# Performance work log

Measured on AMD Instinct MI355X. Metric: run time of the kernel, lower is better.

Reference implementation:

```python
import jax, jax.numpy as jnp
import numpy as np

VX, VY = 0.16, 0.16
PC = (0.0, -39.68, -3.0, 69.12, 39.68, 1.0)
X_OFFSET = VX / 2 + PC[0]
Y_OFFSET = VY / 2 + PC[1]
X_L = int((PC[3] - PC[0]) / VX)   # 432
Y_L = int((PC[4] - PC[1]) / VY)   # 496
C = 64
BN_EPS = 1e-3
LN_EPS = 1e-5


def setup_inputs() -> dict:
    key = jax.random.key(0)
    ks = jax.random.split(key, 16)
    B, PPB, M = 4, 10000, 32
    P = B * PPB
    # unique (x,y) pillar coords per batch, sorted by batch index (matches per-batch loop order)
    rng = np.random.default_rng(0)
    coords = []
    for i in range(B):
        lin = rng.choice(X_L * Y_L, PPB, replace=False)
        coords.append(np.stack([np.full(PPB, i), lin // Y_L, lin % Y_L], axis=1))
    coors_batch = jnp.asarray(np.concatenate(coords, axis=0), dtype=jnp.int32)
    npoints_per_pillar = jax.random.randint(ks[0], (P,), 1, M + 1, dtype=jnp.int32)
    lo = jnp.array([0.5, -39.68, -3.0, 0.0], jnp.float32)
    hi = jnp.array([69.12, 39.68, 1.0, 1.0], jnp.float32)
    pts = lo + jax.random.uniform(ks[1], (P, M, 4), dtype=jnp.float32) * (hi - lo)
    valid = (jnp.arange(M)[None, :] < npoints_per_pillar[:, None])[:, :, None]
    pillars = pts * valid  # zero-padded beyond npoints, as real voxelizers produce
    H_IMG, W_IMG = 192, 640  # half-resolution image feature map
    batch_image_map = jax.random.normal(ks[2], (B, C, H_IMG, W_IMG), dtype=jnp.float32)
    # pinhole-style 3x4 projection with forward-x as depth: u=(cx*x - fx*y)/x, v=(cy*x - fy*z)/x
    fx, fy, cx, cy = 700.0, 700.0, 640.0, 192.0
    calib = jnp.array([[cx, -fx, 0.0, 0.0], [cy, 0.0, -fy, 0.0], [1.0, 0.0, 0.0, 0.0]], jnp.float32)
    batched_calibs = jnp.tile(calib[None], (B, 1, 1)) * (1.0 + 0.01 * jax.random.normal(ks[3], (B, 3, 4)))
    conv_w = 0.1 * jax.random.normal(ks[4], (C, 9), dtype=jnp.float32)
    bn_gamma = 1.0 + 0.1 * jax.random.normal(ks[5], (C,), dtype=jnp.float32)
    bn_beta = 0.1 * jax.random.normal(ks[6], (C,), dtype=jnp.float32)
    bn_mean = 0.1 * jax.random.normal(ks[7], (C,), dtype=jnp.float32)
    bn_var = jax.random.uniform(ks[8], (C,), minval=0.5, maxval=1.5, dtype=jnp.float32)
    g_w1 = 0.1 * jax.random.normal(ks[9], (2 * C, 2 * C), dtype=jnp.float32)
    g_b1 = 0.1 * jax.random.normal(ks[10], (2 * C,), dtype=jnp.float32)
    ln_gamma = 1.0 + 0.1 * jax.random.normal(ks[11], (2 * C,), dtype=jnp.float32)
    ln_beta = 0.1 * jax.random.normal(ks[12], (2 * C,), dtype=jnp.float32)
    g_w2 = 0.1 * jax.random.normal(ks[13], (C, 2 * C), dtype=jnp.float32)
    g_b2 = 0.1 * jax.random.normal(ks[14], (C,), dtype=jnp.float32)
    return dict(pillars=pillars, coors_batch=coors_batch, npoints_per_pillar=npoints_per_pillar,
                batch_image_map=batch_image_map, batched_calibs=batched_calibs, batch_size=B,
                conv_w=conv_w, bn_gamma=bn_gamma, bn_beta=bn_beta, bn_mean=bn_mean, bn_var=bn_var,
                g_w1=g_w1, g_b1=g_b1, ln_gamma=ln_gamma, ln_beta=ln_beta, g_w2=g_w2, g_b2=g_b2)


def reference(pillars, coors_batch, npoints_per_pillar, batch_image_map, batched_calibs, batch_size,
              conv_w, bn_gamma, bn_beta, bn_mean, bn_var, g_w1, g_b1, ln_gamma, ln_beta, g_w2, g_b2):
    P, M, _ = pillars.shape
    npts = npoints_per_pillar.astype(pillars.dtype)
    mean_center = jnp.sum(pillars[:, :, :3], axis=1, keepdims=True) / npts[:, None, None]  # [P,1,3]
    offset_pt_center = pillars[:, :, :3] - mean_center
    cx = coors_batch[:, None, 1:2].astype(pillars.dtype) * VX + X_OFFSET
    cy = coors_batch[:, None, 2:3].astype(pillars.dtype) * VY + Y_OFFSET
    x_off = pillars[:, :, 0:1] - cx
    y_off = pillars[:, :, 1:2] - cy
    # channels 0,1 of the original concat are overwritten with x_off,y_off in-place
    features = jnp.concatenate([x_off, y_off, pillars[:, :, 2:], offset_pt_center, x_off, y_off], axis=-1)  # [P,M,9]
    mask = jnp.arange(M)[None, :] < npoints_per_pillar[:, None]
    features = features * mask[:, :, None]
    # Conv1d(k=1, no bias) + BatchNorm1d(eval) + ReLU (double ReLU in source collapses to one)
    h = jnp.einsum('pmi,ci->pmc', features, conv_w)
    h = (h - bn_mean) * (bn_gamma / jnp.sqrt(bn_var + BN_EPS)) + bn_beta
    h = jax.nn.relu(h)
    pooling_features = jnp.max(h, axis=1)  # [P,C]
    # vectorized image-feature gather (coors sorted by batch idx, so order matches the per-batch loop)
    bidx = coors_batch[:, 0]
    ctr = mean_center[:, 0, :]  # [P,3]
    hom = jnp.concatenate([ctr, jnp.ones((P, 1), ctr.dtype)], axis=-1)  # [P,4]
    proj = jnp.einsum('pij,pj->pi', batched_calibs[bidx], hom)
    depth = proj[:, 2]
    u = proj[:, 0] / depth
    v = proj[:, 1] / depth
    h_img, w_img = batch_image_map.shape[2], batch_image_map.shape[3]
    u = jnp.clip(u / 2, 0, w_img - 1).astype(jnp.int32)
    v = jnp.clip(v / 2, 0, h_img - 1).astype(jnp.int32)
    image_features = batch_image_map.transpose(0, 2, 3, 1)[bidx, v, u]  # [P,C]
    # gated fusion
    cat = jnp.concatenate([pooling_features, image_features], axis=1)  # [P,2C]
    g = cat @ g_w1.T + g_b1
    mu = jnp.mean(g, axis=-1, keepdims=True)
    var = jnp.var(g, axis=-1, keepdims=True)
    g = (g - mu) / jnp.sqrt(var + LN_EPS) * ln_gamma + ln_beta
    g = jax.nn.relu(g)
    gate = jax.nn.sigmoid(g @ g_w2.T + g_b2)  # [P,C]
    gate_features = pooling_features * gate + image_features * (1.0 - gate)
    # scatter to dense BEV canvas [B, x_l, y_l, C] then permute to [B, C, y_l, x_l]
    canvas = jnp.zeros((batch_size, X_L, Y_L, C), dtype=jnp.float32)
    canvas = canvas.at[bidx, coors_batch[:, 1], coors_batch[:, 2]].set(gate_features)
    return canvas.transpose(0, 3, 2, 1)
```

## Files before the change

kernel.cpp:

```cpp
#include <hip/hip_runtime.h>
#include <cfloat>
#include <cmath>

#define XL 432
#define YL 496
#define NCH 64
#define HIMG 192
#define WIMG 640
#define HW (HIMG * WIMG)
#define PTS_M 32

#define WAVES 16
#define TPB (WAVES * 64)
#define PPG 4
#define NBLOCKS 256
#define WPITCH 132

typedef const __attribute__((address_space(1))) void* gas_t;
typedef __attribute__((address_space(3))) void* las_t;

__device__ __forceinline__ void gload_lds16(const float* g, float* l) {
    __builtin_amdgcn_global_load_lds((gas_t)g, (las_t)l, 16, 0, 0);
}

#define RED5(v) { v += __shfl_xor(v, 16); v += __shfl_xor(v, 8); v += __shfl_xor(v, 4); \
                  v += __shfl_xor(v, 2);  v += __shfl_xor(v, 1); }

__global__ void zerofill(float4* __restrict__ o, int n4) {
    int i = blockIdx.x * blockDim.x + threadIdx.x;
    const int st = gridDim.x * blockDim.x;
    const float4 z = make_float4(0.f, 0.f, 0.f, 0.f);
    for (; i < n4; i += st) o[i] = z;
}

__global__ __launch_bounds__(256) void transpose_cl(
    const float* __restrict__ img, float* __restrict__ imgT)
{
    __shared__ float t[64 * 257];
    const int b    = blockIdx.x / (HW / 256);
    const int tile = blockIdx.x % (HW / 256);
    const int hw0  = tile * 256;
    const int tid  = threadIdx.x;

    const float* base = img + (size_t)b * NCH * HW + hw0;
    #pragma unroll 4
    for (int c = 0; c < 64; ++c)
        t[c * 257 + tid] = base[(size_t)c * HW + tid];
    __syncthreads();

    float* ob = imgT + ((size_t)b * HW + hw0) * NCH;
    const int c = tid & 63, r = tid >> 6;
    #pragma unroll 4
    for (int it = 0; it < 64; ++it) {
        const int hw = it * 4 + r;
        ob[hw * 64 + c] = t[c * 257 + hw];
    }
}

template<int MODE>
__global__ __launch_bounds__(TPB, 4) void pillar_compute(
    const float* __restrict__ pillars, const int* __restrict__ coors,
    const int* __restrict__ npp, const float* __restrict__ image,
    const float* __restrict__ calibs, const float* __restrict__ conv_w,
    const float* __restrict__ bng, const float* __restrict__ bnb,
    const float* __restrict__ bnm, const float* __restrict__ bnv,
    const float* __restrict__ w1, const float* __restrict__ b1,
    const float* __restrict__ lng, const float* __restrict__ lnb,
    const float* __restrict__ w2, const float* __restrict__ b2,
    float* __restrict__ feat, int* __restrict__ idxmap,
    float* __restrict__ out, int P)
{
    __shared__ float w1p[128 * WPITCH];
    __shared__ float w2p[64 * WPITCH];
    __shared__ float ws[WAVES][512];

    const int tid  = threadIdx.x;
    const int lane = tid & 63;
    const int wv   = tid >> 6;

    for (int i = tid; i < 128 * 32; i += TPB) {
        const int j = i >> 5, k4 = i & 31;
        ((float4*)(w1p + j * WPITCH))[k4] = ((const float4*)w1)[i];
    }
    for (int i = tid; i < 64 * 32; i += TPB) {
        const int j = i >> 5, k4 = i & 31;
        ((float4*)(w2p + j * WPITCH))[k4] = ((const float4*)w2)[i];
    }
    __syncthreads();

    float cw[9];
    #pragma unroll
    for (int i = 0; i < 9; ++i) cw[i] = conv_w[lane * 9 + i];
    const float s   = bng[lane] / sqrtf(bnv[lane] + 1e-3f);
    const float tch = bnb[lane] - bnm[lane] * s;
    const float As  = (cw[0] + cw[4] + cw[7]) * s;
    const float Bs  = (cw[1] + cw[5] + cw[8]) * s;
    const float Cs  = (cw[2] + cw[6]) * s;
    const float Ds  = cw[3] * s;
    const float w07 = (cw[0] + cw[7]) * s;
    const float w18 = (cw[1] + cw[8]) * s;
    const float w4s = cw[4] * s, w5s = cw[5] * s, w6s = cw[6] * s;

    const float b1a = b1[lane], b1b = b1[lane + 64];
    const float lga = lng[lane], lgb = lng[lane + 64];
    const float lba = lnb[lane], lbb = lnb[lane + 64];
    const float gb2 = b2[lane];

    float* wsw = ws[wv];
    const float4* wsf4 = (const float4*)wsw;
    const float4* w1rA = (const float4*)(w1p + lane * WPITCH);
    const float4* w1rB = (const float4*)(w1p + (lane + 64) * WPITCH);
    const float4* w2r  = (const float4*)(w2p + lane * WPITCH);

    const int ntasks = (P + PPG - 1) / PPG;

    for (int grp = blockIdx.x * WAVES + wv; grp < ntasks; grp += NBLOCKS * WAVES) {
        const int pbase = grp * PPG;
        const bool full = (pbase + PPG <= P);

        asm volatile("s_waitcnt lgkmcnt(0)" ::: "memory");
        if (full) {
            const float* src = pillars + (size_t)pbase * (PTS_M * 4);
            gload_lds16(src + lane * 4, wsw);
            gload_lds16(src + 256 + lane * 4, wsw + 256);
        } else {
            #pragma unroll
            for (int h = 0; h < 2; ++h) {
                const int idx = pbase * PTS_M + h * 64 + lane;
                float4 v = make_float4(0.f, 0.f, 0.f, 0.f);
                if (idx < P * PTS_M) v = ((const float4*)pillars)[idx];
                ((float4*)wsw)[h * 64 + lane] = v;
            }
        }

        int bbv[PPG], ixv[PPG], iyv[PPG], nv[PPG];
        #pragma unroll
        for (int pp = 0; pp < PPG; ++pp) {
            const int p = pbase + pp;
            if (p < P) {
                bbv[pp] = coors[p * 3]; ixv[pp] = coors[p * 3 + 1];
                iyv[pp] = coors[p * 3 + 2]; nv[pp] = npp[p];
            } else { bbv[pp] = 0; ixv[pp] = 0; iyv[pp] = 0; nv[pp] = 1; }
        }

        asm volatile("s_waitcnt vmcnt(0) lgkmcnt(0)" ::: "memory");

        const float4 qa = wsf4[lane];
        const float4 qb = wsf4[64 + lane];
        float ax = qa.x, ay = qa.y, az = qa.z;
        float bx = qb.x, by = qb.y, bz = qb.z;
        RED5(ax) RED5(ay) RED5(az)
        RED5(bx) RED5(by) RED5(bz)
        const float axo = __shfl_xor(ax, 32), ayo = __shfl_xor(ay, 32), azo = __shfl_xor(az, 32);
        const float bxo = __shfl_xor(bx, 32), byo = __shfl_xor(by, 32), bzo = __shfl_xor(bz, 32);
        const bool lo = lane < 32;
        float mx[PPG], my[PPG], mz[PPG];
        {
            const float f0 = 1.f / (float)nv[0], f1 = 1.f / (float)nv[1];
            const float f2 = 1.f / (float)nv[2], f3 = 1.f / (float)nv[3];
            mx[0] = (lo ? ax : axo) * f0;  mx[1] = (lo ? axo : ax) * f1;
            my[0] = (lo ? ay : ayo) * f0;  my[1] = (lo ? ayo : ay) * f1;
            mz[0] = (lo ? az : azo) * f0;  mz[1] = (lo ? azo : az) * f1;
            mx[2] = (lo ? bx : bxo) * f2;  mx[3] = (lo ? bxo : bx) * f3;
            my[2] = (lo ? by : byo) * f2;  my[3] = (lo ? byo : by) * f3;
            mz[2] = (lo ? bz : bzo) * f2;  mz[3] = (lo ? bzo : bz) * f3;
        }

        float img[PPG], Es[PPG];
        #pragma unroll
        for (int pp = 0; pp < PPG; ++pp) {
            const float* cb = calibs + bbv[pp] * 12;
            const float pr0 = cb[0]*mx[pp] + cb[1]*my[pp] + cb[2]*mz[pp] + cb[3];
            const float pr1 = cb[4]*mx[pp] + cb[5]*my[pp] + cb[6]*mz[pp] + cb[7];
            const float pr2 = cb[8]*mx[pp] + cb[9]*my[pp] + cb[10]*mz[pp] + cb[11];
            float uf = (pr0 / pr2) * 0.5f;
            float vf = (pr1 / pr2) * 0.5f;
            uf = fminf(fmaxf(uf, 0.f), (float)(WIMG - 1));
            vf = fminf(fmaxf(vf, 0.f), (float)(HIMG - 1));
            const int u = (int)uf, v = (int)vf;
            if (MODE == 2) {
                img[pp] = image[((size_t)bbv[pp] * HW + (size_t)v * WIMG + u) * NCH + lane];
            } else {
                img[pp] = image[(((size_t)(bbv[pp] * NCH + lane)) * HIMG + v) * WIMG + u];
            }
            const float cxp = (float)ixv[pp] * 0.16f + 0.08f;
            const float cyp = (float)iyv[pp] * 0.16f + (-39.6f);
            Es[pp] = tch - (cxp * w07 + cyp * w18 + mx[pp] * w4s + my[pp] * w5s + mz[pp] * w6s);
        }

        float pooled[PPG];
        #pragma unroll
        for (int pp = 0; pp < PPG; ++pp) {
            const int n = nv[pp];
            float p0 = (n < PTS_M) ? tch : -FLT_MAX;
            float p1 = -FLT_MAX, p2 = -FLT_MAX, p3 = -FLT_MAX;
            #pragma unroll
            for (int m = 0; m < PTS_M; m += 4) {
                const float4 q0 = wsf4[pp * 32 + m];
                const float4 q1 = wsf4[pp * 32 + m + 1];
                const float4 q2 = wsf4[pp * 32 + m + 2];
                const float4 q3 = wsf4[pp * 32 + m + 3];
                const float h0 = Es[pp] + q0.x*As + q0.y*Bs + q0.z*Cs + q0.w*Ds;
                const float h1 = Es[pp] + q1.x*As + q1.y*Bs + q1.z*Cs + q1.w*Ds;
                const float h2 = Es[pp] + q2.x*As + q2.y*Bs + q2.z*Cs + q2.w*Ds;
                const float h3 = Es[pp] + q3.x*As + q3.y*Bs + q3.z*Cs + q3.w*Ds;
                p0 = fmaxf(p0, (m     < n) ? h0 : -FLT_MAX);
                p1 = fmaxf(p1, (m + 1 < n) ? h1 : -FLT_MAX);
                p2 = fmaxf(p2, (m + 2 < n) ? h2 : -FLT_MAX);
                p3 = fmaxf(p3, (m + 3 < n) ? h3 : -FLT_MAX);
            }
            pooled[pp] = fmaxf(fmaxf(fmaxf(p0, p1), fmaxf(p2, p3)), 0.f);
        }

        #pragma unroll
        for (int pp = 0; pp < PPG; ++pp) {
            wsw[pp * 128 + lane]      = pooled[pp];
            wsw[pp * 128 + 64 + lane] = img[pp];
        }
        asm volatile("s_waitcnt lgkmcnt(0)" ::: "memory");

        float accA[PPG], accB[PPG];
        #pragma unroll
        for (int pp = 0; pp < PPG; ++pp) { accA[pp] = b1a; accB[pp] = b1b; }
        #pragma unroll 4
        for (int k4 = 0; k4 < 32; ++k4) {
            const float4 wa = w1rA[k4];
            const float4 wb = w1rB[k4];
            #pragma unroll
            for (int pp = 0; pp < PPG; ++pp) {
                const float4 cv = wsf4[pp * 32 + k4];
                accA[pp] += cv.x*wa.x + cv.y*wa.y + cv.z*wa.z + cv.w*wa.w;
                accB[pp] += cv.x*wb.x + cv.y*wb.y + cv.z*wb.z + cv.w*wb.w;
            }
        }

        float sum[PPG], sq[PPG];
        #pragma unroll
        for (int pp = 0; pp < PPG; ++pp) {
            sum[pp] = accA[pp] + accB[pp];
            sq[pp]  = accA[pp]*accA[pp] + accB[pp]*accB[pp];
        }
        #pragma unroll
        for (int d = 32; d; d >>= 1) {
            #pragma unroll
            for (int pp = 0; pp < PPG; ++pp) {
                sum[pp] += __shfl_xor(sum[pp], d);
                sq[pp]  += __shfl_xor(sq[pp], d);
            }
        }
        #pragma unroll
        for (int pp = 0; pp < PPG; ++pp) {
            const float mu  = sum[pp] * (1.f / 128.f);
            const float var = sq[pp] * (1.f / 128.f) - mu * mu;
            const float inv = 1.f / sqrtf(var + 1e-5f);
            const float g0 = (accA[pp] - mu) * inv * lga + lba;
            const float g1 = (accB[pp] - mu) * inv * lgb + lbb;
            wsw[pp * 128 + lane]      = fmaxf(g0, 0.f);
            wsw[pp * 128 + 64 + lane] = fmaxf(g1, 0.f);
        }
        asm volatile("s_waitcnt lgkmcnt(0)" ::: "memory");

        float ac2[PPG];
        #pragma unroll
        for (int pp = 0; pp < PPG; ++pp) ac2[pp] = gb2;
        #pragma unroll 4
        for (int k4 = 0; k4 < 32; ++k4) {
            const float4 w = w2r[k4];
            #pragma unroll
            for (int pp = 0; pp < PPG; ++pp) {
                const float4 gv = wsf4[pp * 32 + k4];
                ac2[pp] += gv.x*w.x + gv.y*w.y + gv.z*w.z + gv.w*w.w;
            }
        }
        #pragma unroll
        for (int pp = 0; pp < PPG; ++pp) {
            const int p = pbase + pp;
            if (p >= P) continue;
            const float gate = 1.f / (1.f + expf(-ac2[pp]));
            const float gf = pooled[pp] * gate + img[pp] * (1.f - gate);
            if (MODE == 0) {
                out[(((bbv[pp] * NCH) + lane) * YL + iyv[pp]) * XL + ixv[pp]] = gf;
            } else {
                feat[(size_t)p * NCH + lane] = gf;
                if (lane == 0)
                    idxmap[(bbv[pp] * YL + iyv[pp]) * XL + ixv[pp]] = p + 1;
            }
        }
    }
}

__global__ __launch_bounds__(256) void canvas_build(
    const float* __restrict__ feat, const int* __restrict__ idxmap,
    float4* __restrict__ out)
{
    __shared__ int idxrow[XL];
    const int by = blockIdx.x;
    const int b = by / YL, y = by % YL;
    const int* irow = idxmap + (size_t)by * XL;
    for (int i = threadIdx.x; i < XL; i += 256) idxrow[i] = irow[i];
    __syncthreads();

    const int NF4 = XL / 4;
    for (int t = threadIdx.x; t < NCH * NF4; t += 256) {
        const int c = t / NF4, x4 = t - c * NF4;
        const int i0 = idxrow[x4*4+0], i1 = idxrow[x4*4+1];
        const int i2 = idxrow[x4*4+2], i3 = idxrow[x4*4+3];
        float4 o = make_float4(0.f, 0.f, 0.f, 0.f);
        if (i0) o.x = feat[(size_t)(i0-1) * NCH + c];
        if (i1) o.y = feat[(size_t)(i1-1) * NCH + c];
        if (i2) o.z = feat[(size_t)(i2-1) * NCH + c];
        if (i3) o.w = feat[(size_t)(i3-1) * NCH + c];
        out[((size_t)(b * NCH + c) * YL + y) * NF4 + x4] = o;
    }
}

extern "C" void kernel_launch(void* const* d_in, const int* in_sizes, int n_in,
                              void* d_out, int out_size, void* d_ws, size_t ws_size,
                              hipStream_t stream)
{
    const float* pillars = (const float*)d_in[0];
    const int*   coors   = (const int*)d_in[1];
    const int*   npp     = (const int*)d_in[2];
    const float* image   = (const float*)d_in[3];
    const float* calibs  = (const float*)d_in[4];
    const float* conv_w  = (const float*)d_in[6];
    const float* bng     = (const float*)d_in[7];
    const float* bnb     = (const float*)d_in[8];
    const float* bnm     = (const float*)d_in[9];
    const float* bnv     = (const float*)d_in[10];
    const float* w1      = (const float*)d_in[11];
    const float* b1      = (const float*)d_in[12];
    const float* lng     = (const float*)d_in[13];
    const float* lnb     = (const float*)d_in[14];
    const float* w2      = (const float*)d_in[15];
    const float* b2      = (const float*)d_in[16];
    float* out = (float*)d_out;
    const int P = in_sizes[0] / (PTS_M * 4);
    const int B = in_sizes[3] / (NCH * HW);

    const size_t featBytes = (size_t)P * NCH * sizeof(float);
    const size_t idxBytes  = (size_t)B * YL * XL * sizeof(int);
    const size_t imgTBytes = (size_t)B * HW * NCH * sizeof(float);

    if (ws_size >= featBytes + idxBytes + imgTBytes) {
        float* feat   = (float*)d_ws;
        int*   idxmap = (int*)((char*)d_ws + featBytes);
        float* imgT   = (float*)((char*)d_ws + featBytes + idxBytes);
        zerofill<<<dim3(880), dim3(256), 0, stream>>>((float4*)idxmap, (int)(idxBytes / 16));
        transpose_cl<<<dim3(B * (HW / 256)), dim3(256), 0, stream>>>(image, imgT);
        pillar_compute<2><<<dim3(NBLOCKS), dim3(TPB), 0, stream>>>(
            pillars, coors, npp, imgT, calibs, conv_w, bng, bnb, bnm, bnv,
            w1, b1, lng, lnb, w2, b2, feat, idxmap, nullptr, P);
        canvas_build<<<dim3(B * YL), dim3(256), 0, stream>>>(feat, idxmap, (float4*)d_out);
    } else if (ws_size >= featBytes + idxBytes) {
        float* feat   = (float*)d_ws;
        int*   idxmap = (int*)((char*)d_ws + featBytes);
        zerofill<<<dim3(880), dim3(256), 0, stream>>>((float4*)idxmap, (int)(idxBytes / 16));
        pillar_compute<1><<<dim3(NBLOCKS), dim3(TPB), 0, stream>>>(
            pillars, coors, npp, image, calibs, conv_w, bng, bnb, bnm, bnv,
            w1, b1, lng, lnb, w2, b2, feat, idxmap, nullptr, P);
        canvas_build<<<dim3(B * YL), dim3(256), 0, stream>>>(feat, idxmap, (float4*)d_out);
    } else {
        zerofill<<<dim3(2048), dim3(256), 0, stream>>>((float4*)d_out, out_size / 4);
        pillar_compute<0><<<dim3(NBLOCKS), dim3(TPB), 0, stream>>>(
            pillars, coors, npp, image, calibs, conv_w, bng, bnb, bnm, bnv,
            w1, b1, lng, lnb, w2, b2, nullptr, nullptr, out, P);
    }
}
```

Measured before the change: 210.5 us.

## Fuse zerofill, transpose, pillar compute and canvas build into one cooperative kernel

```diff
diff --git a/kernel.cpp b/kernel.cpp
--- a/kernel.cpp
+++ b/kernel.cpp
@@ -1,6 +1,9 @@
 #include <hip/hip_runtime.h>
+#include <hip/hip_cooperative_groups.h>
 #include <cfloat>
 #include <cmath>
+
+namespace cg = cooperative_groups;
 
 #define XL 432
 #define YL 496
@@ -26,6 +29,335 @@
 #define RED5(v) { v += __shfl_xor(v, 16); v += __shfl_xor(v, 8); v += __shfl_xor(v, 4); \
                   v += __shfl_xor(v, 2);  v += __shfl_xor(v, 1); }
 
+
+struct ChanConst {
+    float As, Bs, Cs, Ds, w07, w18, w4s, w5s, w6s, tch;
+    float b1a, b1b, lga, lgb, lba, lbb, gb2;
+};
+
+__device__ __forceinline__ ChanConst load_chan_consts(
+    int lane, const float* conv_w, const float* bng, const float* bnb,
+    const float* bnm, const float* bnv, const float* b1, const float* lng,
+    const float* lnb, const float* b2)
+{
+    ChanConst cc;
+    float cw[9];
+    #pragma unroll
+    for (int i = 0; i < 9; ++i) cw[i] = conv_w[lane * 9 + i];
+    const float s = bng[lane] / sqrtf(bnv[lane] + 1e-3f);
+    cc.tch = bnb[lane] - bnm[lane] * s;
+    cc.As  = (cw[0] + cw[4] + cw[7]) * s;
+    cc.Bs  = (cw[1] + cw[5] + cw[8]) * s;
+    cc.Cs  = (cw[2] + cw[6]) * s;
+    cc.Ds  = cw[3] * s;
+    cc.w07 = (cw[0] + cw[7]) * s;
+    cc.w18 = (cw[1] + cw[8]) * s;
+    cc.w4s = cw[4] * s; cc.w5s = cw[5] * s; cc.w6s = cw[6] * s;
+    cc.b1a = b1[lane];  cc.b1b = b1[lane + 64];
+    cc.lga = lng[lane]; cc.lgb = lng[lane + 64];
+    cc.lba = lnb[lane]; cc.lbb = lnb[lane + 64];
+    cc.gb2 = b2[lane];
+    return cc;
+}
+
+template<int MODE>
+__device__ __forceinline__ void pillar_group(
+    int grp, int P, int lane, float* wsw,
+    const float* __restrict__ pillars, const int* __restrict__ coors,
+    const int* __restrict__ npp, const float* __restrict__ image,
+    const float* __restrict__ calibs, const ChanConst& cc,
+    const float4* w1rA, const float4* w1rB, const float4* w2r,
+    float* __restrict__ feat, int* __restrict__ idxmap, float* __restrict__ out)
+{
+    const float4* wsf4 = (const float4*)wsw;
+    const int pbase = grp * PPG;
+    const bool full = (pbase + PPG <= P);
+
+    asm volatile("s_waitcnt lgkmcnt(0)" ::: "memory");
+    if (full) {
+        const float* src = pillars + (size_t)pbase * (PTS_M * 4);
+        gload_lds16(src + lane * 4, wsw);
+        gload_lds16(src + 256 + lane * 4, wsw + 256);
+    } else {
+        #pragma unroll
+        for (int h = 0; h < 2; ++h) {
+            const int idx = pbase * PTS_M + h * 64 + lane;
+            float4 v = make_float4(0.f, 0.f, 0.f, 0.f);
+            if (idx < P * PTS_M) v = ((const float4*)pillars)[idx];
+            ((float4*)wsw)[h * 64 + lane] = v;
+        }
+    }
+
+    int bbv[PPG], ixv[PPG], iyv[PPG], nv[PPG];
+    #pragma unroll
+    for (int pp = 0; pp < PPG; ++pp) {
+        const int p = pbase + pp;
+        if (p < P) {
+            bbv[pp] = coors[p * 3]; ixv[pp] = coors[p * 3 + 1];
+            iyv[pp] = coors[p * 3 + 2]; nv[pp] = npp[p];
+        } else { bbv[pp] = 0; ixv[pp] = 0; iyv[pp] = 0; nv[pp] = 1; }
+    }
+
+    asm volatile("s_waitcnt vmcnt(0) lgkmcnt(0)" ::: "memory");
+
+    const float4 qa = wsf4[lane];
+    const float4 qb = wsf4[64 + lane];
+    float ax = qa.x, ay = qa.y, az = qa.z;
+    float bx = qb.x, by = qb.y, bz = qb.z;
+    RED5(ax) RED5(ay) RED5(az)
+    RED5(bx) RED5(by) RED5(bz)
+    const float axo = __shfl_xor(ax, 32), ayo = __shfl_xor(ay, 32), azo = __shfl_xor(az, 32);
+    const float bxo = __shfl_xor(bx, 32), byo = __shfl_xor(by, 32), bzo = __shfl_xor(bz, 32);
+    const bool lo = lane < 32;
+    float mx[PPG], my[PPG], mz[PPG];
+    {
+        const float f0 = 1.f / (float)nv[0], f1 = 1.f / (float)nv[1];
+        const float f2 = 1.f / (float)nv[2], f3 = 1.f / (float)nv[3];
+        mx[0] = (lo ? ax : axo) * f0;  mx[1] = (lo ? axo : ax) * f1;
+        my[0] = (lo ? ay : ayo) * f0;  my[1] = (lo ? ayo : ay) * f1;
+        mz[0] = (lo ? az : azo) * f0;  mz[1] = (lo ? azo : az) * f1;
+        mx[2] = (lo ? bx : bxo) * f2;  mx[3] = (lo ? bxo : bx) * f3;
+        my[2] = (lo ? by : byo) * f2;  my[3] = (lo ? byo : by) * f3;
+        mz[2] = (lo ? bz : bzo) * f2;  mz[3] = (lo ? bzo : bz) * f3;
+    }
+
+    float img[PPG], Es[PPG];
+    #pragma unroll
+    for (int pp = 0; pp < PPG; ++pp) {
+        const float* cb = calibs + bbv[pp] * 12;
+        const float pr0 = cb[0]*mx[pp] + cb[1]*my[pp] + cb[2]*mz[pp] + cb[3];
+        const float pr1 = cb[4]*mx[pp] + cb[5]*my[pp] + cb[6]*mz[pp] + cb[7];
+        const float pr2 = cb[8]*mx[pp] + cb[9]*my[pp] + cb[10]*mz[pp] + cb[11];
+        float uf = (pr0 / pr2) * 0.5f;
+        float vf = (pr1 / pr2) * 0.5f;
+        uf = fminf(fmaxf(uf, 0.f), (float)(WIMG - 1));
+        vf = fminf(fmaxf(vf, 0.f), (float)(HIMG - 1));
+        const int u = (int)uf, v = (int)vf;
+        if (MODE == 2) {
+            img[pp] = image[((size_t)bbv[pp] * HW + (size_t)v * WIMG + u) * NCH + lane];
+        } else {
+            img[pp] = image[(((size_t)(bbv[pp] * NCH + lane)) * HIMG + v) * WIMG + u];
+        }
+        const float cxp = (float)ixv[pp] * 0.16f + 0.08f;
+        const float cyp = (float)iyv[pp] * 0.16f + (-39.6f);
+        Es[pp] = cc.tch - (cxp * cc.w07 + cyp * cc.w18 + mx[pp] * cc.w4s + my[pp] * cc.w5s + mz[pp] * cc.w6s);
+    }
+
+    float pooled[PPG];
+    #pragma unroll
+    for (int pp = 0; pp < PPG; ++pp) {
+        const int n = nv[pp];
+        float p0 = (n < PTS_M) ? cc.tch : -FLT_MAX;
+        float p1 = -FLT_MAX, p2 = -FLT_MAX, p3 = -FLT_MAX;
+        #pragma unroll
+        for (int m = 0; m < PTS_M; m += 4) {
+            const float4 q0 = wsf4[pp * 32 + m];
+            const float4 q1 = wsf4[pp * 32 + m + 1];
+            const float4 q2 = wsf4[pp * 32 + m + 2];
+            const float4 q3 = wsf4[pp * 32 + m + 3];
+            const float h0 = Es[pp] + q0.x*cc.As + q0.y*cc.Bs + q0.z*cc.Cs + q0.w*cc.Ds;
+            const float h1 = Es[pp] + q1.x*cc.As + q1.y*cc.Bs + q1.z*cc.Cs + q1.w*cc.Ds;
+            const float h2 = Es[pp] + q2.x*cc.As + q2.y*cc.Bs + q2.z*cc.Cs + q2.w*cc.Ds;
+            const float h3 = Es[pp] + q3.x*cc.As + q3.y*cc.Bs + q3.z*cc.Cs + q3.w*cc.Ds;
+            p0 = fmaxf(p0, (m     < n) ? h0 : -FLT_MAX);
+            p1 = fmaxf(p1, (m + 1 < n) ? h1 : -FLT_MAX);
+            p2 = fmaxf(p2, (m + 2 < n) ? h2 : -FLT_MAX);
+            p3 = fmaxf(p3, (m + 3 < n) ? h3 : -FLT_MAX);
+        }
+        pooled[pp] = fmaxf(fmaxf(fmaxf(p0, p1), fmaxf(p2, p3)), 0.f);
+    }
+
+    #pragma unroll
+    for (int pp = 0; pp < PPG; ++pp) {
+        wsw[pp * 128 + lane]      = pooled[pp];
+        wsw[pp * 128 + 64 + lane] = img[pp];
+    }
+    asm volatile("s_waitcnt lgkmcnt(0)" ::: "memory");
+
+    float accA[PPG], accB[PPG];
+    #pragma unroll
+    for (int pp = 0; pp < PPG; ++pp) { accA[pp] = cc.b1a; accB[pp] = cc.b1b; }
+    #pragma unroll 4
+    for (int k4 = 0; k4 < 32; ++k4) {
+        const float4 wa = w1rA[k4];
+        const float4 wb = w1rB[k4];
+        #pragma unroll
+        for (int pp = 0; pp < PPG; ++pp) {
+            const float4 cv = wsf4[pp * 32 + k4];
+            accA[pp] += cv.x*wa.x + cv.y*wa.y + cv.z*wa.z + cv.w*wa.w;
+            accB[pp] += cv.x*wb.x + cv.y*wb.y + cv.z*wb.z + cv.w*wb.w;
+        }
+    }
+
+    float sum[PPG], sq[PPG];
+    #pragma unroll
+    for (int pp = 0; pp < PPG; ++pp) {
+        sum[pp] = accA[pp] + accB[pp];
+        sq[pp]  = accA[pp]*accA[pp] + accB[pp]*accB[pp];
+    }
+    #pragma unroll
+    for (int d = 32; d; d >>= 1) {
+        #pragma unroll
+        for (int pp = 0; pp < PPG; ++pp) {
+            sum[pp] += __shfl_xor(sum[pp], d);
+            sq[pp]  += __shfl_xor(sq[pp], d);
+        }
+    }
+    #pragma unroll
+    for (int pp = 0; pp < PPG; ++pp) {
+        const float mu  = sum[pp] * (1.f / 128.f);
+        const float var = sq[pp] * (1.f / 128.f) - mu * mu;
+        const float inv = 1.f / sqrtf(var + 1e-5f);
+        const float g0 = (accA[pp] - mu) * inv * cc.lga + cc.lba;
+        const float g1 = (accB[pp] - mu) * inv * cc.lgb + cc.lbb;
+        wsw[pp * 128 + lane]      = fmaxf(g0, 0.f);
+        wsw[pp * 128 + 64 + lane] = fmaxf(g1, 0.f);
+    }
+    asm volatile("s_waitcnt lgkmcnt(0)" ::: "memory");
+
+    float ac2[PPG];
+    #pragma unroll
+    for (int pp = 0; pp < PPG; ++pp) ac2[pp] = cc.gb2;
+    #pragma unroll 4
+    for (int k4 = 0; k4 < 32; ++k4) {
+        const float4 w = w2r[k4];
+        #pragma unroll
+        for (int pp = 0; pp < PPG; ++pp) {
+            const float4 gv = wsf4[pp * 32 + k4];
+            ac2[pp] += gv.x*w.x + gv.y*w.y + gv.z*w.z + gv.w*w.w;
+        }
+    }
+    #pragma unroll
+    for (int pp = 0; pp < PPG; ++pp) {
+        const int p = pbase + pp;
+        if (p >= P) continue;
+        const float gate = 1.f / (1.f + expf(-ac2[pp]));
+        const float gf = pooled[pp] * gate + img[pp] * (1.f - gate);
+        if (MODE == 0) {
+            out[(((bbv[pp] * NCH) + lane) * YL + iyv[pp]) * XL + ixv[pp]] = gf;
+        } else {
+            feat[(size_t)p * NCH + lane] = gf;
+            if (lane == 0)
+                idxmap[(bbv[pp] * YL + iyv[pp]) * XL + ixv[pp]] = p + 1;
+        }
+    }
+}
+
+__global__ __launch_bounds__(TPB, 1) void pillar_mega(
+    const float* __restrict__ pillars, const int* __restrict__ coors,
+    const int* __restrict__ npp, const float* __restrict__ image,
+    const float* __restrict__ calibs, const float* __restrict__ conv_w,
+    const float* __restrict__ bng, const float* __restrict__ bnb,
+    const float* __restrict__ bnm, const float* __restrict__ bnv,
+    const float* __restrict__ w1, const float* __restrict__ b1,
+    const float* __restrict__ lng, const float* __restrict__ lnb,
+    const float* __restrict__ w2, const float* __restrict__ b2,
+    float* __restrict__ feat, int* __restrict__ idxmap,
+    float* __restrict__ imgT, float* __restrict__ out, int P, int B)
+{
+    __shared__ float w1p[128 * WPITCH];
+    __shared__ float w2p[64 * WPITCH];
+    __shared__ float ws[WAVES][512];
+
+    cg::grid_group grid = cg::this_grid();
+    const int tid  = threadIdx.x;
+    const int lane = tid & 63;
+    const int wv   = tid >> 6;
+    const int bid  = blockIdx.x;
+
+    {
+        const int n4 = (B * YL * XL) / 4;
+        int4* o = (int4*)idxmap;
+        const int4 z = make_int4(0, 0, 0, 0);
+        for (int i = bid * TPB + tid; i < n4; i += NBLOCKS * TPB) o[i] = z;
+    }
+
+    {
+        float* tt = w1p;
+        const int NT = B * (HW / 256);
+        for (int tile = bid; tile < NT; tile += NBLOCKS) {
+            const int b   = tile / (HW / 256);
+            const int px0 = (tile % (HW / 256)) * 256;
+            const float4* base4 = (const float4*)(image + (size_t)b * NCH * HW + px0);
+            __syncthreads();
+            #pragma unroll 2
+            for (int i = tid; i < 64 * 64; i += TPB) {
+                const int c = i >> 6, f4 = i & 63;
+                const float4 v = base4[(size_t)c * (HW / 4) + f4];
+                tt[c * 257 + f4]       = v.x;
+                tt[c * 257 + f4 + 64]  = v.y;
+                tt[c * 257 + f4 + 128] = v.z;
+                tt[c * 257 + f4 + 192] = v.w;
+            }
+            __syncthreads();
+            float4* ob4 = (float4*)(imgT + ((size_t)b * HW + px0) * NCH);
+            #pragma unroll 2
+            for (int i = tid; i < 256 * 16; i += TPB) {
+                const int c4 = i & 15, hw = i >> 4;
+                const int off = (hw >> 2) + 64 * (hw & 3);
+                float4 o;
+                o.x = tt[(4 * c4 + 0) * 257 + off];
+                o.y = tt[(4 * c4 + 1) * 257 + off];
+                o.z = tt[(4 * c4 + 2) * 257 + off];
+                o.w = tt[(4 * c4 + 3) * 257 + off];
+                ob4[(size_t)hw * 16 + c4] = o;
+            }
+        }
+    }
+    __threadfence();
+    grid.sync();
+
+    {
+        for (int i = tid; i < 128 * 32; i += TPB) {
+            const int j = i >> 5, k4 = i & 31;
+            ((float4*)(w1p + j * WPITCH))[k4] = ((const float4*)w1)[i];
+        }
+        for (int i = tid; i < 64 * 32; i += TPB) {
+            const int j = i >> 5, k4 = i & 31;
+            ((float4*)(w2p + j * WPITCH))[k4] = ((const float4*)w2)[i];
+        }
+        __syncthreads();
+
+        const ChanConst cc = load_chan_consts(lane, conv_w, bng, bnb, bnm, bnv, b1, lng, lnb, b2);
+        float* wsw = ws[wv];
+        const float4* w1rA = (const float4*)(w1p + lane * WPITCH);
+        const float4* w1rB = (const float4*)(w1p + (lane + 64) * WPITCH);
+        const float4* w2r  = (const float4*)(w2p + lane * WPITCH);
+
+        const int ntasks = (P + PPG - 1) / PPG;
+        for (int grp = bid * WAVES + wv; grp < ntasks; grp += NBLOCKS * WAVES)
+            pillar_group<2>(grp, P, lane, wsw, pillars, coors, npp, imgT, calibs,
+                            cc, w1rA, w1rB, w2r, feat, idxmap, nullptr);
+    }
+    __threadfence();
+    grid.sync();
+
+    {
+        int* idxrow = (int*)ws;
+        const int NROW = B * YL;
+        const int NF4  = XL / 4;
+        for (int by = bid; by < NROW; by += NBLOCKS) {
+            const int b = by / YL, y = by % YL;
+            __syncthreads();
+            if (tid < 108) ((int4*)idxrow)[tid] = ((const int4*)(idxmap + (size_t)by * XL))[tid];
+            __syncthreads();
+            float4* orow = (float4*)(out) + (size_t)b * NCH * YL * NF4 + (size_t)y * NF4;
+            for (int t = tid; t < NCH * NF4; t += TPB) {
+                const int c = t / NF4, x4 = t - c * NF4;
+                const int i0 = idxrow[x4*4+0], i1 = idxrow[x4*4+1];
+                const int i2 = idxrow[x4*4+2], i3 = idxrow[x4*4+3];
+                float4 o = make_float4(0.f, 0.f, 0.f, 0.f);
+                if (i0) o.x = feat[(size_t)(i0-1) * NCH + c];
+                if (i1) o.y = feat[(size_t)(i1-1) * NCH + c];
+                if (i2) o.z = feat[(size_t)(i2-1) * NCH + c];
+                if (i3) o.w = feat[(size_t)(i3-1) * NCH + c];
+                orow[(size_t)c * YL * NF4 + x4] = o;
+            }
+        }
+    }
+}
+
+
 __global__ void zerofill(float4* __restrict__ o, int n4) {
     int i = blockIdx.x * blockDim.x + threadIdx.x;
     const int st = gridDim.x * blockDim.x;
@@ -41,13 +373,11 @@
     const int tile = blockIdx.x % (HW / 256);
     const int hw0  = tile * 256;
     const int tid  = threadIdx.x;
-
     const float* base = img + (size_t)b * NCH * HW + hw0;
     #pragma unroll 4
     for (int c = 0; c < 64; ++c)
         t[c * 257 + tid] = base[(size_t)c * HW + tid];
     __syncthreads();
-
     float* ob = imgT + ((size_t)b * HW + hw0) * NCH;
     const int c = tid & 63, r = tid >> 6;
     #pragma unroll 4
@@ -58,7 +388,7 @@
 }
 
 template<int MODE>
-__global__ __launch_bounds__(TPB, 4) void pillar_compute(
+__global__ __launch_bounds__(TPB, 1) void pillar_compute(
     const float* __restrict__ pillars, const int* __restrict__ coors,
     const int* __restrict__ npp, const float* __restrict__ image,
     const float* __restrict__ calibs, const float* __restrict__ conv_w,
@@ -73,11 +403,9 @@
     __shared__ float w1p[128 * WPITCH];
     __shared__ float w2p[64 * WPITCH];
     __shared__ float ws[WAVES][512];
-
     const int tid  = threadIdx.x;
     const int lane = tid & 63;
     const int wv   = tid >> 6;
-
     for (int i = tid; i < 128 * 32; i += TPB) {
         const int j = i >> 5, k4 = i & 31;
         ((float4*)(w1p + j * WPITCH))[k4] = ((const float4*)w1)[i];
@@ -87,206 +415,15 @@
         ((float4*)(w2p + j * WPITCH))[k4] = ((const float4*)w2)[i];
     }
     __syncthreads();
-
-    float cw[9];
-    #pragma unroll
-    for (int i = 0; i < 9; ++i) cw[i] = conv_w[lane * 9 + i];
-    const float s   = bng[lane] / sqrtf(bnv[lane] + 1e-3f);
-    const float tch = bnb[lane] - bnm[lane] * s;
-    const float As  = (cw[0] + cw[4] + cw[7]) * s;
-    const float Bs  = (cw[1] + cw[5] + cw[8]) * s;
-    const float Cs  = (cw[2] + cw[6]) * s;
-    const float Ds  = cw[3] * s;
-    const float w07 = (cw[0] + cw[7]) * s;
-    const float w18 = (cw[1] + cw[8]) * s;
-    const float w4s = cw[4] * s, w5s = cw[5] * s, w6s = cw[6] * s;
-
-    const float b1a = b1[lane], b1b = b1[lane + 64];
-    const float lga = lng[lane], lgb = lng[lane + 64];
-    const float lba = lnb[lane], lbb = lnb[lane + 64];
-    const float gb2 = b2[lane];
-
+    const ChanConst cc = load_chan_consts(lane, conv_w, bng, bnb, bnm, bnv, b1, lng, lnb, b2);
     float* wsw = ws[wv];
-    const float4* wsf4 = (const float4*)wsw;
     const float4* w1rA = (const float4*)(w1p + lane * WPITCH);
     const float4* w1rB = (const float4*)(w1p + (lane + 64) * WPITCH);
     const float4* w2r  = (const float4*)(w2p + lane * WPITCH);
-
     const int ntasks = (P + PPG - 1) / PPG;
-
-    for (int grp = blockIdx.x * WAVES + wv; grp < ntasks; grp += NBLOCKS * WAVES) {
-        const int pbase = grp * PPG;
-        const bool full = (pbase + PPG <= P);
-
-        asm volatile("s_waitcnt lgkmcnt(0)" ::: "memory");
-        if (full) {
-            const float* src = pillars + (size_t)pbase * (PTS_M * 4);
-            gload_lds16(src + lane * 4, wsw);
-            gload_lds16(src + 256 + lane * 4, wsw + 256);
-        } else {
-            #pragma unroll
-            for (int h = 0; h < 2; ++h) {
-                const int idx = pbase * PTS_M + h * 64 + lane;
-                float4 v = make_float4(0.f, 0.f, 0.f, 0.f);
-                if (idx < P * PTS_M) v = ((const float4*)pillars)[idx];
-                ((float4*)wsw)[h * 64 + lane] = v;
-            }
-        }
-
-        int bbv[PPG], ixv[PPG], iyv[PPG], nv[PPG];
-        #pragma unroll
-        for (int pp = 0; pp < PPG; ++pp) {
-            const int p = pbase + pp;
-            if (p < P) {
-                bbv[pp] = coors[p * 3]; ixv[pp] = coors[p * 3 + 1];
-                iyv[pp] = coors[p * 3 + 2]; nv[pp] = npp[p];
-            } else { bbv[pp] = 0; ixv[pp] = 0; iyv[pp] = 0; nv[pp] = 1; }
-        }
-
-        asm volatile("s_waitcnt vmcnt(0) lgkmcnt(0)" ::: "memory");
-
-        const float4 qa = wsf4[lane];
-        const float4 qb = wsf4[64 + lane];
-        float ax = qa.x, ay = qa.y, az = qa.z;
-        float bx = qb.x, by = qb.y, bz = qb.z;
-        RED5(ax) RED5(ay) RED5(az)
-        RED5(bx) RED5(by) RED5(bz)
-        const float axo = __shfl_xor(ax, 32), ayo = __shfl_xor(ay, 32), azo = __shfl_xor(az, 32);
-        const float bxo = __shfl_xor(bx, 32), byo = __shfl_xor(by, 32), bzo = __shfl_xor(bz, 32);
-        const bool lo = lane < 32;
-        float mx[PPG], my[PPG], mz[PPG];
-        {
-            const float f0 = 1.f / (float)nv[0], f1 = 1.f / (float)nv[1];
-            const float f2 = 1.f / (float)nv[2], f3 = 1.f / (float)nv[3];
-            mx[0] = (lo ? ax : axo) * f0;  mx[1] = (lo ? axo : ax) * f1;
-            my[0] = (lo ? ay : ayo) * f0;  my[1] = (lo ? ayo : ay) * f1;
-            mz[0] = (lo ? az : azo) * f0;  mz[1] = (lo ? azo : az) * f1;
-            mx[2] = (lo ? bx : bxo) * f2;  mx[3] = (lo ? bxo : bx) * f3;
-            my[2] = (lo ? by : byo) * f2;  my[3] = (lo ? byo : by) * f3;
-            mz[2] = (lo ? bz : bzo) * f2;  mz[3] = (lo ? bzo : bz) * f3;
-        }
-
-        float img[PPG], Es[PPG];
-        #pragma unroll
-        for (int pp = 0; pp < PPG; ++pp) {
-            const float* cb = calibs + bbv[pp] * 12;
-            const float pr0 = cb[0]*mx[pp] + cb[1]*my[pp] + cb[2]*mz[pp] + cb[3];
-            const float pr1 = cb[4]*mx[pp] + cb[5]*my[pp] + cb[6]*mz[pp] + cb[7];
-            const float pr2 = cb[8]*mx[pp] + cb[9]*my[pp] + cb[10]*mz[pp] + cb[11];
-            float uf = (pr0 / pr2) * 0.5f;
-            float vf = (pr1 / pr2) * 0.5f;
-            uf = fminf(fmaxf(uf, 0.f), (float)(WIMG - 1));
-            vf = fminf(fmaxf(vf, 0.f), (float)(HIMG - 1));
-            const int u = (int)uf, v = (int)vf;
-            if (MODE == 2) {
-                img[pp] = image[((size_t)bbv[pp] * HW + (size_t)v * WIMG + u) * NCH + lane];
-            } else {
-                img[pp] = image[(((size_t)(bbv[pp] * NCH + lane)) * HIMG + v) * WIMG + u];
-            }
-            const float cxp = (float)ixv[pp] * 0.16f + 0.08f;
-            const float cyp = (float)iyv[pp] * 0.16f + (-39.6f);
-            Es[pp] = tch - (cxp * w07 + cyp * w18 + mx[pp] * w4s + my[pp] * w5s + mz[pp] * w6s);
-        }
-
-        float pooled[PPG];
-        #pragma unroll
-        for (int pp = 0; pp < PPG; ++pp) {
-            const int n = nv[pp];
-            float p0 = (n < PTS_M) ? tch : -FLT_MAX;
-            float p1 = -FLT_MAX, p2 = -FLT_MAX, p3 = -FLT_MAX;
-            #pragma unroll
-            for (int m = 0; m < PTS_M; m += 4) {
-                const float4 q0 = wsf4[pp * 32 + m];
-                const float4 q1 = wsf4[pp * 32 + m + 1];
-                const float4 q2 = wsf4[pp * 32 + m + 2];
-                const float4 q3 = wsf4[pp * 32 + m + 3];
-                const float h0 = Es[pp] + q0.x*As + q0.y*Bs + q0.z*Cs + q0.w*Ds;
-                const float h1 = Es[pp] + q1.x*As + q1.y*Bs + q1.z*Cs + q1.w*Ds;
-                const float h2 = Es[pp] + q2.x*As + q2.y*Bs + q2.z*Cs + q2.w*Ds;
-                const float h3 = Es[pp] + q3.x*As + q3.y*Bs + q3.z*Cs + q3.w*Ds;
-                p0 = fmaxf(p0, (m     < n) ? h0 : -FLT_MAX);
-                p1 = fmaxf(p1, (m + 1 < n) ? h1 : -FLT_MAX);
-                p2 = fmaxf(p2, (m + 2 < n) ? h2 : -FLT_MAX);
-                p3 = fmaxf(p3, (m + 3 < n) ? h3 : -FLT_MAX);
-            }
-            pooled[pp] = fmaxf(fmaxf(fmaxf(p0, p1), fmaxf(p2, p3)), 0.f);
-        }
-
-        #pragma unroll
-        for (int pp = 0; pp < PPG; ++pp) {
-            wsw[pp * 128 + lane]      = pooled[pp];
-            wsw[pp * 128 + 64 + lane] = img[pp];
-        }
-        asm volatile("s_waitcnt lgkmcnt(0)" ::: "memory");
-
-        float accA[PPG], accB[PPG];
-        #pragma unroll
-        for (int pp = 0; pp < PPG; ++pp) { accA[pp] = b1a; accB[pp] = b1b; }
-        #pragma unroll 4
-        for (int k4 = 0; k4 < 32; ++k4) {
-            const float4 wa = w1rA[k4];
-            const float4 wb = w1rB[k4];
-            #pragma unroll
-            for (int pp = 0; pp < PPG; ++pp) {
-                const float4 cv = wsf4[pp * 32 + k4];
-                accA[pp] += cv.x*wa.x + cv.y*wa.y + cv.z*wa.z + cv.w*wa.w;
-                accB[pp] += cv.x*wb.x + cv.y*wb.y + cv.z*wb.z + cv.w*wb.w;
-            }
-        }
-
-        float sum[PPG], sq[PPG];
-        #pragma unroll
-        for (int pp = 0; pp < PPG; ++pp) {
-            sum[pp] = accA[pp] + accB[pp];
-            sq[pp]  = accA[pp]*accA[pp] + accB[pp]*accB[pp];
-        }
-        #pragma unroll
-        for (int d = 32; d; d >>= 1) {
-            #pragma unroll
-            for (int pp = 0; pp < PPG; ++pp) {
-                sum[pp] += __shfl_xor(sum[pp], d);
-                sq[pp]  += __shfl_xor(sq[pp], d);
-            }
-        }
-        #pragma unroll
-        for (int pp = 0; pp < PPG; ++pp) {
-            const float mu  = sum[pp] * (1.f / 128.f);
-            const float var = sq[pp] * (1.f / 128.f) - mu * mu;
-            const float inv = 1.f / sqrtf(var + 1e-5f);
-            const float g0 = (accA[pp] - mu) * inv * lga + lba;
-            const float g1 = (accB[pp] - mu) * inv * lgb + lbb;
-            wsw[pp * 128 + lane]      = fmaxf(g0, 0.f);
-            wsw[pp * 128 + 64 + lane] = fmaxf(g1, 0.f);
-        }
-        asm volatile("s_waitcnt lgkmcnt(0)" ::: "memory");
-
-        float ac2[PPG];
-        #pragma unroll
-        for (int pp = 0; pp < PPG; ++pp) ac2[pp] = gb2;
-        #pragma unroll 4
-        for (int k4 = 0; k4 < 32; ++k4) {
-            const float4 w = w2r[k4];
-            #pragma unroll
-            for (int pp = 0; pp < PPG; ++pp) {
-                const float4 gv = wsf4[pp * 32 + k4];
-                ac2[pp] += gv.x*w.x + gv.y*w.y + gv.z*w.z + gv.w*w.w;
-            }
-        }
-        #pragma unroll
-        for (int pp = 0; pp < PPG; ++pp) {
-            const int p = pbase + pp;
-            if (p >= P) continue;
-            const float gate = 1.f / (1.f + expf(-ac2[pp]));
-            const float gf = pooled[pp] * gate + img[pp] * (1.f - gate);
-            if (MODE == 0) {
-                out[(((bbv[pp] * NCH) + lane) * YL + iyv[pp]) * XL + ixv[pp]] = gf;
-            } else {
-                feat[(size_t)p * NCH + lane] = gf;
-                if (lane == 0)
-                    idxmap[(bbv[pp] * YL + iyv[pp]) * XL + ixv[pp]] = p + 1;
-            }
-        }
-    }
+    for (int grp = blockIdx.x * WAVES + wv; grp < ntasks; grp += NBLOCKS * WAVES)
+        pillar_group<MODE>(grp, P, lane, wsw, pillars, coors, npp, image, calibs,
+                           cc, w1rA, w1rB, w2r, feat, idxmap, out);
 }
 
 __global__ __launch_bounds__(256) void canvas_build(
@@ -299,7 +436,6 @@
     const int* irow = idxmap + (size_t)by * XL;
     for (int i = threadIdx.x; i < XL; i += 256) idxrow[i] = irow[i];
     __syncthreads();
-
     const int NF4 = XL / 4;
     for (int t = threadIdx.x; t < NCH * NF4; t += 256) {
         const int c = t / NF4, x4 = t - c * NF4;
@@ -313,6 +449,7 @@
         out[((size_t)(b * NCH + c) * YL + y) * NF4 + x4] = o;
     }
 }
+
 
 extern "C" void kernel_launch(void* const* d_in, const int* in_sizes, int n_in,
                               void* d_out, int out_size, void* d_ws, size_t ws_size,
@@ -346,6 +483,21 @@
         float* feat   = (float*)d_ws;
         int*   idxmap = (int*)((char*)d_ws + featBytes);
         float* imgT   = (float*)((char*)d_ws + featBytes + idxBytes);
+
+        int Pv = P, Bv = B;
+        void* args[] = {
+            (void*)&pillars, (void*)&coors, (void*)&npp, (void*)&image,
+            (void*)&calibs, (void*)&conv_w, (void*)&bng, (void*)&bnb,
+            (void*)&bnm, (void*)&bnv, (void*)&w1, (void*)&b1,
+            (void*)&lng, (void*)&lnb, (void*)&w2, (void*)&b2,
+            (void*)&feat, (void*)&idxmap, (void*)&imgT, (void*)&out,
+            (void*)&Pv, (void*)&Bv
+        };
+        hipError_t e = hipLaunchCooperativeKernel(
+            reinterpret_cast<const void*>(pillar_mega),
+            dim3(NBLOCKS), dim3(TPB), args, 0, stream);
+        if (e == hipSuccess) return;
+
         zerofill<<<dim3(880), dim3(256), 0, stream>>>((float4*)idxmap, (int)(idxBytes / 16));
         transpose_cl<<<dim3(B * (HW / 256)), dim3(256), 0, stream>>>(image, imgT);
         pillar_compute<2><<<dim3(NBLOCKS), dim3(TPB), 0, stream>>>(
```

Result: slower. 466.1 us (+121.5%).
